# Kernel optimization log

Measured on AMD Instinct MI355X. Metric: run time of the kernel, lower is better.

The kernel has to match this reference:

```python
import jax, jax.numpy as jnp
import numpy as np

V_IN = 32000
V_OUT = 32000
E = 1024
H = 1024
B = 16
T = 512


def _lstm_layer(xs, Wih, Whh, bih, bhh):
    # xs: [T, B, in_dim]; PyTorch gate order: i, f, g, o (each size H)
    gx = jnp.einsum('tbi,gi->tbg', xs, Wih) + bih + bhh  # [T, B, 4H]

    def step(carry, g_t):
        h, c = carry
        g = g_t + h @ Whh.T  # [B, 4H]
        i, f, gg, o = jnp.split(g, 4, axis=-1)
        i = jax.nn.sigmoid(i)
        f = jax.nn.sigmoid(f)
        gg = jnp.tanh(gg)
        o = jax.nn.sigmoid(o)
        c = f * c + i * gg
        h = o * jnp.tanh(c)
        return (h, c), h

    h0 = jnp.zeros((xs.shape[1], Whh.shape[1]), dtype=xs.dtype)
    c0 = jnp.zeros_like(h0)
    _, hs = jax.lax.scan(step, (h0, c0), gx)
    return hs  # [T, B, H]


def setup_inputs() -> dict:
    key = jax.random.key(0)
    ks = jax.random.split(key, 12)
    s_e = 1.0  # nn.Embedding default init is N(0,1)
    s_l = 1.0 / np.sqrt(H)  # LSTM/Linear uniform bound 1/sqrt(H)

    def u(k, shape):
        return jax.random.uniform(k, shape, jnp.float32, -s_l, s_l)

    return {
        'x': jax.random.randint(ks[0], (B, T), 0, V_IN),
        'emb': jax.random.normal(ks[1], (V_IN, E), jnp.float32) * s_e,
        'W_ih0': u(ks[2], (4 * H, E)),
        'W_hh0': u(ks[3], (4 * H, H)),
        'b_ih0': u(ks[4], (4 * H,)),
        'b_hh0': u(ks[5], (4 * H,)),
        'W_ih1': u(ks[6], (4 * H, H)),
        'W_hh1': u(ks[7], (4 * H, H)),
        'b_ih1': u(ks[8], (4 * H,)),
        'b_hh1': u(ks[9], (4 * H,)),
        'W_out': u(ks[10], (V_OUT, H)),
        'b_out': u(ks[11], (V_OUT,)),
    }


def reference(x, emb, W_ih0, W_hh0, b_ih0, b_hh0, W_ih1, W_hh1, b_ih1, b_hh1, W_out, b_out):
    # embedding + permute to [T, B, E]
    out = emb[x].transpose(1, 0, 2)
    out = _lstm_layer(out, W_ih0, W_hh0, b_ih0, b_hh0)
    out = _lstm_layer(out, W_ih1, W_hh1, b_ih1, b_hh1)
    logits = jnp.einsum('tbh,oh->tbo', out, W_out) + b_out
    return logits.transpose(1, 0, 2)  # [B, T, V_OUT]
```

## Files before the change

kernel.cpp:

```cpp
#include <hip/hip_runtime.h>
#include <cstdint>
#include <cstddef>

typedef __bf16 bf16;
typedef float f32x4 __attribute__((ext_vector_type(4)));
typedef bf16 bf16x8 __attribute__((ext_vector_type(8)));
typedef bf16 bf16x4 __attribute__((ext_vector_type(4)));

#define AS1 __attribute__((address_space(1)))
#define AS3 __attribute__((address_space(3)))

__device__ __forceinline__ void gload_lds16(const void* g, void* l) {
  __builtin_amdgcn_global_load_lds((AS1 void*)g, (AS3 void*)l, 16, 0, 0);
}

#define RING 8
#define FLAG_WORDS 1024

__global__ __launch_bounds__(256) void init_misc(
    const float* __restrict__ bih0, const float* __restrict__ bhh0,
    const float* __restrict__ bih1, const float* __restrict__ bhh1,
    float* __restrict__ bsum0, float* __restrict__ bsum1, unsigned* __restrict__ flags) {
  int i = blockIdx.x * 256 + threadIdx.x;
  if (i < 4096) {
    bsum0[i] = bih0[i] + bhh0[i];
    bsum1[i] = bih1[i] + bhh1[i];
  }
  if (i < FLAG_WORDS) flags[i] = 0u;
}

__global__ __launch_bounds__(256) void embed_gather(
    const int* __restrict__ x, const float* __restrict__ emb, bf16* __restrict__ xe, int T) {
  int row = blockIdx.x;
  int t = row >> 4, b = row & 15;
  int tok = x[b * T + t];
  int cix = threadIdx.x << 2;
  f32x4 v = *(const f32x4*)(emb + ((size_t)tok << 10) + cix);
  bf16x4 o;
  for (int j = 0; j < 4; ++j) o[j] = (bf16)v[j];
  *(bf16x4*)(xe + ((size_t)row << 10) + cix) = o;
}

template <int OUTMODE>
__global__ __launch_bounds__(256) void gemm_bf16(
    const bf16* __restrict__ A, const float* __restrict__ Bw,
    const float* __restrict__ bias, float* __restrict__ C,
    int M, int N, int K, int Tdim) {
  __shared__ bf16 aL[2][128 * 32];
  __shared__ bf16 bL[2][128 * 32];
  const int tid = threadIdx.x;
  const int l = tid & 63, w = tid >> 6;
  const int nbm = M >> 7;
  const int bm = blockIdx.x % nbm;
  const int bn = blockIdx.x / nbm;
  const int wr = (w >> 1) << 6, wc = (w & 1) << 6;
  const int NT = K >> 5;
  const int r16 = l & 15, kq = l >> 4;

  f32x4 acc[4][4];
  for (int m = 0; m < 4; ++m)
    for (int n = 0; n < 4; ++n) acc[m][n] = (f32x4){0.f, 0.f, 0.f, 0.f};

  for (int i = 0; i < 2; ++i) {
    int lin = tid + (i << 8);
    int r = lin >> 2, s = lin & 3, c = s ^ (r & 3);
    gload_lds16(A + (size_t)((bm << 7) + r) * K + (c << 3), &aL[0][lin << 3]);
  }
  for (int i = 0; i < 2; ++i) {
    int lin = tid + (i << 8);
    int r = lin >> 2, c = lin & 3;
    const float* src = Bw + (size_t)((bn << 7) + r) * K + (c << 3);
    f32x4 v0 = *(const f32x4*)src;
    f32x4 v1 = *(const f32x4*)(src + 4);
    bf16x8 o;
    for (int j = 0; j < 4; ++j) { o[j] = (bf16)v0[j]; o[j + 4] = (bf16)v1[j]; }
    *(bf16x8*)&bL[0][(r << 5) + ((c ^ (r & 3)) << 3)] = o;
  }
  __syncthreads();

  for (int kt = 0; kt < NT; ++kt) {
    const int cur = kt & 1;
    const bool pf = (kt + 1 < NT);
    f32x4 bv0[2], bv1[2];
    int br_[2], bs_[2];
    if (pf) {
      for (int i = 0; i < 2; ++i) {
        int lin = tid + (i << 8);
        int r = lin >> 2, s = lin & 3, c = s ^ (r & 3);
        gload_lds16(A + (size_t)((bm << 7) + r) * K + ((kt + 1) << 5) + (c << 3),
                    &aL[cur ^ 1][lin << 3]);
      }
      for (int i = 0; i < 2; ++i) {
        int lin = tid + (i << 8);
        int r = lin >> 2, c = lin & 3;
        const float* src = Bw + (size_t)((bn << 7) + r) * K + ((kt + 1) << 5) + (c << 3);
        bv0[i] = *(const f32x4*)src;
        bv1[i] = *(const f32x4*)(src + 4);
        br_[i] = r;
        bs_[i] = c ^ (r & 3);
      }
    }
    bf16x8 af[4], bfr[4];
    for (int m = 0; m < 4; ++m) {
      int row = wr + (m << 4) + r16;
      int ch = kq ^ (row & 3);
      af[m] = *(const bf16x8*)&aL[cur][(row << 5) + (ch << 3)];
    }
    for (int n = 0; n < 4; ++n) {
      int row = wc + (n << 4) + r16;
      int ch = kq ^ (row & 3);
      bfr[n] = *(const bf16x8*)&bL[cur][(row << 5) + (ch << 3)];
    }
    for (int m = 0; m < 4; ++m)
      for (int n = 0; n < 4; ++n)
        acc[m][n] = __builtin_amdgcn_mfma_f32_16x16x32_bf16(af[m], bfr[n], acc[m][n], 0, 0, 0);
    if (pf) {
      for (int i = 0; i < 2; ++i) {
        bf16x8 o;
        for (int j = 0; j < 4; ++j) { o[j] = (bf16)bv0[i][j]; o[j + 4] = (bf16)bv1[i][j]; }
        *(bf16x8*)&bL[cur ^ 1][(br_[i] << 5) + (bs_[i] << 3)] = o;
      }
    }
    __syncthreads();
  }

  float bvv[4];
  for (int n = 0; n < 4; ++n) bvv[n] = bias[(bn << 7) + wc + (n << 4) + r16];
  for (int m = 0; m < 4; ++m) {
    int Rbase = (bm << 7) + wr + (m << 4) + (kq << 2);
    for (int r = 0; r < 4; ++r) {
      int R = Rbase + r;
      size_t rowoff;
      if (OUTMODE == 0) {
        rowoff = (size_t)R * N;
      } else {
        int tt = R >> 4, bb = R & 15;
        rowoff = ((size_t)bb * Tdim + tt) * N;
      }
      for (int n = 0; n < 4; ++n)
        C[rowoff + (bn << 7) + wc + (n << 4) + r16] = acc[m][n][r] + bvv[n];
    }
  }
}

__global__ __launch_bounds__(256, 1) void lstm_pipe3(
    const float* __restrict__ gx,
    const float* __restrict__ Whh0,
    const float* __restrict__ Wih1,
    const float* __restrict__ Whh1,
    const float* __restrict__ bsum1,
    bf16* __restrict__ hs0t,
    bf16* __restrict__ hs1t,
    float* __restrict__ gx1,
    bf16* __restrict__ hs1rm,
    unsigned* __restrict__ flags,
    int T) {
  __shared__ bf16 wlds[4][16 * 1024];
  __shared__ unsigned short hb[4][64];
  __shared__ unsigned tokv[4];
  const int tid = threadIdx.x;
  const int l = tid & 63, w = tid >> 6;
  const int bid = blockIdx.x;
  const int r16 = l & 15, kq = l >> 4;
  unsigned* const fL0 = flags;
  unsigned* const fB = flags + 256;
  unsigned* const fL1 = flags + 512;
  const int typ = bid >> 6;
  const int lb = bid & 63;
  const int widx = lb * 4 + w;
  const int colbase = lb * 16 + w * 4;

  {
    const float* Wsrc = (typ == 0) ? Whh0 : ((typ == 1) ? Wih1 : Whh1);
    for (int it = 0; it < 32; ++it) {
      int lin = it * 64 + l;
      int row = lin >> 7, cs = lin & 127, c = cs ^ (row & 7);
      const float* s = Wsrc + (size_t)((row >> 2) * 1024 + colbase + (row & 3)) * 1024 + c * 8;
      f32x4 v0 = *(const f32x4*)s;
      f32x4 v1 = *(const f32x4*)(s + 4);
      bf16x8 o;
      for (int j = 0; j < 4; ++j) { o[j] = (bf16)v0[j]; o[j + 4] = (bf16)v1[j]; }
      *(bf16x8*)&wlds[w][row * 1024 + cs * 8] = o;
    }
  }
  if (tid < 4) tokv[tid] = 0;
  __syncthreads();

  const int gcol = (r16 >> 2) * 1024 + colbase + (r16 & 3);
  const int b0s = (r16 >> 2) & 1, b1s = (r16 >> 3) & 1;

  auto pollq = [&](unsigned* arr, unsigned tgt) {
    unsigned* q = arr + w * 64 + (l & 15) * 4;
    for (;;) {
      unsigned a0 = __hip_atomic_load(q + 0, __ATOMIC_RELAXED, __HIP_MEMORY_SCOPE_AGENT);
      unsigned a1 = __hip_atomic_load(q + 1, __ATOMIC_RELAXED, __HIP_MEMORY_SCOPE_AGENT);
      unsigned a2 = __hip_atomic_load(q + 2, __ATOMIC_RELAXED, __HIP_MEMORY_SCOPE_AGENT);
      unsigned a3 = __hip_atomic_load(q + 3, __ATOMIC_RELAXED, __HIP_MEMORY_SCOPE_AGENT);
      if (__all(a0 >= tgt && a1 >= tgt && a2 >= tgt && a3 >= tgt)) break;
      __builtin_amdgcn_s_sleep(2);
    }
    volatile unsigned* tk = tokv;
    if (l == 0) tk[w] = tgt;
    while (tk[0] < tgt || tk[1] < tgt || tk[2] < tgt || tk[3] < tgt) {
    }
    asm volatile("" ::: "memory");
  };
  auto poll1 = [&](unsigned* p, unsigned tgt) {
    while (__hip_atomic_load(p, __ATOMIC_RELAXED, __HIP_MEMORY_SCOPE_AGENT) < tgt)
      __builtin_amdgcn_s_sleep(2);
    asm volatile("" ::: "memory");
  };
  auto chain = [&](const bf16* plane) -> f32x4 {
    f32x4 acc = (f32x4){0.f, 0.f, 0.f, 0.f};
    const char* hp = (const char*)plane;
#pragma unroll 8
    for (int kk = 0; kk < 32; ++kk) {
      int tl = kk * 8 + kq * 2;
      unsigned long long lo = *(const unsigned long long*)(hp + tl * 128 + r16 * 8);
      unsigned long long hi = *(const unsigned long long*)(hp + tl * 128 + 128 + r16 * 8);
      union { struct { unsigned long long a, b; } u; bf16x8 v; } A;
      A.u.a = lo;
      A.u.b = hi;
      bf16x8 Bf = *(const bf16x8*)&wlds[w][r16 * 1024 + (((kk * 4 + kq) ^ (r16 & 7)) << 3)];
      acc = __builtin_amdgcn_mfma_f32_16x16x32_bf16(A.v, Bf, acc, 0, 0, 0);
    }
    return acc;
  };

  if (typ == 1) {
    const float bsv = bsum1[gcol];
    unsigned* const myflag = fB + widx;
    unsigned* const partner = fL1 + widx;
    for (int t = 0; t < T; ++t) {
      if (t >= RING) poll1(partner, (unsigned)(t - RING + 1));
      pollq(fL0, (unsigned)(t + 1));
      f32x4 acc = chain(hs0t + (size_t)t * 16384);
      for (int r = 0; r < 4; ++r) acc[r] += bsv;
      float* dst = gx1 + (size_t)(t & (RING - 1)) * 65536 + widx * 256 + r16 * 16 + kq * 4;
      asm volatile("global_store_dwordx4 %0, %1, off sc0 sc1" ::"v"(dst), "v"(acc) : "memory");
      asm volatile("s_waitcnt vmcnt(0)" ::: "memory");
      if (l == 0)
        __hip_atomic_store(myflag, (unsigned)(t + 1), __ATOMIC_RELAXED, __HIP_MEMORY_SCOPE_AGENT);
    }
    return;
  }

  float cst[4] = {0.f, 0.f, 0.f, 0.f};
  unsigned* const myflag = (typ == 0) ? (fL0 + widx) : (fL1 + widx);
  unsigned* const bpartner = fB + widx;
  bf16* const houts = (typ == 0) ? hs0t : hs1t;

  for (int t = 0; t < T; ++t) {
    float gxv[4];
    if (typ == 0) {
      for (int r = 0; r < 4; ++r)
        gxv[r] = gx[(size_t)(t * 16 + kq * 4 + r) * 4096 + gcol];
    }
    if (typ == 0) {
      if (t > 0) pollq(fL0, (unsigned)t);
    } else {
      poll1(bpartner, (unsigned)(t + 1));
      if (t > 0) pollq(fL1, (unsigned)t);
    }
    f32x4 acc = (f32x4){0.f, 0.f, 0.f, 0.f};
    if (t > 0) acc = chain(houts + (size_t)(t - 1) * 16384);
    if (typ == 0) {
      for (int r = 0; r < 4; ++r) acc[r] += gxv[r];
    } else {
      const float* gp = gx1 + (size_t)(t & (RING - 1)) * 65536 + widx * 256 + r16 * 16 + kq * 4;
      f32x4 g1;
      asm volatile("global_load_dwordx4 %0, %1, off sc0 sc1\ns_waitcnt vmcnt(0)"
                   : "=v"(g1) : "v"(gp) : "memory");
      for (int r = 0; r < 4; ++r) acc[r] += g1[r];
    }
    float hv[4];
    for (int r = 0; r < 4; ++r) {
      float own = acc[r];
      float p4 = __shfl_xor(own, 4, 64);
      float ev = b0s ? p4 : own;
      float ov = b0s ? own : p4;
      float ev8 = __shfl_xor(ev, 8, 64);
      float ov8 = __shfl_xor(ov, 8, 64);
      float xi = b1s ? ev8 : ev;
      float xf = b1s ? ov8 : ov;
      float xg = b1s ? ev : ev8;
      float xo = b1s ? ov : ov8;
      float ig = 1.f / (1.f + __expf(-xi));
      float fg = 1.f / (1.f + __expf(-xf));
      float eg = __expf(2.f * xg);
      float gv = 1.f - 2.f / (eg + 1.f);
      float og = 1.f / (1.f + __expf(-xo));
      cst[r] = fg * cst[r] + ig * gv;
      float ec = __expf(2.f * cst[r]);
      float th = 1.f - 2.f / (ec + 1.f);
      hv[r] = og * th;
    }
    if (r16 < 4) {
      volatile unsigned short* hbp = hb[w];
      for (int r = 0; r < 4; ++r) {
        bf16 hbv = (bf16)hv[r];
        hbp[(kq * 4 + r) * 4 + r16] = __builtin_bit_cast(unsigned short, hbv);
      }
    }
    unsigned long long rowv = 0;
    if (l < 16) rowv = *(volatile unsigned long long*)&hb[w][l * 4];
    if (l < 16) {
      char* dst = (char*)houts + (size_t)t * 32768 + widx * 128 + l * 8;
      asm volatile("global_store_dwordx2 %0, %1, off sc0 sc1" ::"v"(dst), "v"(rowv) : "memory");
    }
    asm volatile("s_waitcnt vmcnt(0)" ::: "memory");
    if (l == 0)
      __hip_atomic_store(myflag, (unsigned)(t + 1), __ATOMIC_RELAXED, __HIP_MEMORY_SCOPE_AGENT);
    if (typ == 1 + 1 && l < 16) {
      *(unsigned long long*)((char*)hs1rm + ((size_t)(t * 16 + l) * 1024 + colbase) * 2) = rowv;
    }
  }
}

extern "C" void kernel_launch(void* const* d_in, const int* in_sizes, int n_in,
                              void* d_out, int out_size, void* d_ws, size_t ws_size,
                              hipStream_t stream) {
  const int* x = (const int*)d_in[0];
  const float* emb = (const float*)d_in[1];
  const float* Wih0 = (const float*)d_in[2];
  const float* Whh0 = (const float*)d_in[3];
  const float* bih0 = (const float*)d_in[4];
  const float* bhh0 = (const float*)d_in[5];
  const float* Wih1 = (const float*)d_in[6];
  const float* Whh1 = (const float*)d_in[7];
  const float* bih1 = (const float*)d_in[8];
  const float* bhh1 = (const float*)d_in[9];
  const float* Wout = (const float*)d_in[10];
  const float* bout = (const float*)d_in[11];

  const int T = 512, H = 1024, V = 32000;
  const int M = T * 16;
  const size_t bfb = (size_t)M * H * 2;
  const size_t out_bytes = (size_t)out_size * 4;

  char* p = (char*)d_ws;
  bf16* hs1rm = (bf16*)p;         p += bfb;
  float* bsum0 = (float*)p;       p += 4096 * 4;
  float* bsum1 = (float*)p;       p += 4096 * 4;
  unsigned* flags = (unsigned*)p; p += FLAG_WORDS * 4;

  float* gx = (float*)d_out;
  float* gx1 = (float*)((char*)d_out + (512ull << 20));
  char* tail = (char*)d_out + out_bytes - 3 * bfb;
  bf16* xe = (bf16*)tail;
  bf16* hs0t = (bf16*)(tail + bfb);
  bf16* hs1t = (bf16*)(tail + 2 * bfb);

  init_misc<<<64, 256, 0, stream>>>(bih0, bhh0, bih1, bhh1, bsum0, bsum1, flags);
  embed_gather<<<M, 256, 0, stream>>>(x, emb, xe, T);
  gemm_bf16<0><<<(M / 128) * (4096 / 128), 256, 0, stream>>>(xe, Wih0, bsum0, gx, M, 4096, H, 0);
  lstm_pipe3<<<192, 256, 0, stream>>>(gx, Whh0, Wih1, Whh1, bsum1, hs0t, hs1t, gx1, hs1rm,
                                      flags, T);
  gemm_bf16<1><<<(M / 128) * (V / 128), 256, 0, stream>>>(hs1rm, Wout, bout, (float*)d_out,
                                                          M, V, H, T);
}
```

Before: 5.294 ms.

## Fuse embedding gather into input GEMM and pre-convert W_out to bf16

The separate embedding gather kernel is removed; the first GEMM now reads token rows from the embedding table directly and converts them to bf16 while staging. When workspace allows, W_out is converted to bf16 once, so the output projection loads it straight into LDS with async global-to-LDS copies instead of fp32 register loads plus conversion. The projection GEMM also uses a grouped block ordering to improve L2 reuse and nontemporal stores for the large logits output. The added conversion pass costs extra memory traffic, and the fused gather gives up the async A-loads in the first GEMM.

```diff
diff --git a/kernel.cpp b/kernel.cpp
--- a/kernel.cpp
+++ b/kernel.cpp
@@ -5,7 +5,6 @@
 typedef __bf16 bf16;
 typedef float f32x4 __attribute__((ext_vector_type(4)));
 typedef bf16 bf16x8 __attribute__((ext_vector_type(8)));
-typedef bf16 bf16x4 __attribute__((ext_vector_type(4)));
 
 #define AS1 __attribute__((address_space(1)))
 #define AS3 __attribute__((address_space(3)))
@@ -29,77 +28,58 @@
   if (i < FLAG_WORDS) flags[i] = 0u;
 }
 
-__global__ __launch_bounds__(256) void embed_gather(
-    const int* __restrict__ x, const float* __restrict__ emb, bf16* __restrict__ xe, int T) {
-  int row = blockIdx.x;
-  int t = row >> 4, b = row & 15;
-  int tok = x[b * T + t];
-  int cix = threadIdx.x << 2;
-  f32x4 v = *(const f32x4*)(emb + ((size_t)tok << 10) + cix);
-  bf16x4 o;
-  for (int j = 0; j < 4; ++j) o[j] = (bf16)v[j];
-  *(bf16x4*)(xe + ((size_t)row << 10) + cix) = o;
-}
-
-template <int OUTMODE>
-__global__ __launch_bounds__(256) void gemm_bf16(
-    const bf16* __restrict__ A, const float* __restrict__ Bw,
-    const float* __restrict__ bias, float* __restrict__ C,
-    int M, int N, int K, int Tdim) {
-  __shared__ bf16 aL[2][128 * 32];
-  __shared__ bf16 bL[2][128 * 32];
+__global__ __launch_bounds__(256) void wout_cvt(
+    const float* __restrict__ W, bf16* __restrict__ o) {
+  size_t i = ((size_t)blockIdx.x * 256 + threadIdx.x) * 8;
+  f32x4 v0 = *(const f32x4*)(W + i);
+  f32x4 v1 = *(const f32x4*)(W + i + 4);
+  bf16x8 r;
+  for (int j = 0; j < 4; ++j) { r[j] = (bf16)v0[j]; r[j + 4] = (bf16)v1[j]; }
+  *(bf16x8*)(o + i) = r;
+}
+
+__global__ __launch_bounds__(256) void gemm_emb(
+    const int* __restrict__ x, const float* __restrict__ emb,
+    const float* __restrict__ Wih0, const float* __restrict__ bsum0,
+    float* __restrict__ C) {
+  __shared__ bf16 aL[2][4096];
+  __shared__ bf16 bL[2][4096];
   const int tid = threadIdx.x;
   const int l = tid & 63, w = tid >> 6;
-  const int nbm = M >> 7;
-  const int bm = blockIdx.x % nbm;
-  const int bn = blockIdx.x / nbm;
+  const int bm = blockIdx.x & 63;
+  const int bn = blockIdx.x >> 6;
   const int wr = (w >> 1) << 6, wc = (w & 1) << 6;
-  const int NT = K >> 5;
   const int r16 = l & 15, kq = l >> 4;
 
   f32x4 acc[4][4];
   for (int m = 0; m < 4; ++m)
     for (int n = 0; n < 4; ++n) acc[m][n] = (f32x4){0.f, 0.f, 0.f, 0.f};
 
-  for (int i = 0; i < 2; ++i) {
-    int lin = tid + (i << 8);
-    int r = lin >> 2, s = lin & 3, c = s ^ (r & 3);
-    gload_lds16(A + (size_t)((bm << 7) + r) * K + (c << 3), &aL[0][lin << 3]);
-  }
-  for (int i = 0; i < 2; ++i) {
-    int lin = tid + (i << 8);
-    int r = lin >> 2, c = lin & 3;
-    const float* src = Bw + (size_t)((bn << 7) + r) * K + (c << 3);
-    f32x4 v0 = *(const f32x4*)src;
-    f32x4 v1 = *(const f32x4*)(src + 4);
-    bf16x8 o;
-    for (int j = 0; j < 4; ++j) { o[j] = (bf16)v0[j]; o[j + 4] = (bf16)v1[j]; }
-    *(bf16x8*)&bL[0][(r << 5) + ((c ^ (r & 3)) << 3)] = o;
-  }
+  auto stage = [&](int kt, int buf) {
+    for (int i = 0; i < 2; ++i) {
+      int lin = tid + (i << 8);
+      int r = lin >> 2, c = lin & 3;
+      int rg = (bm << 7) + r;
+      int tok = x[((rg & 15) << 9) + (rg >> 4)];
+      const float* sa = emb + ((size_t)tok << 10) + (kt << 5) + (c << 3);
+      f32x4 a0 = *(const f32x4*)sa;
+      f32x4 a1 = *(const f32x4*)(sa + 4);
+      bf16x8 oa;
+      for (int j = 0; j < 4; ++j) { oa[j] = (bf16)a0[j]; oa[j + 4] = (bf16)a1[j]; }
+      *(bf16x8*)&aL[buf][(r << 5) + ((c ^ (r & 3)) << 3)] = oa;
+      const float* sb = Wih0 + (size_t)((bn << 7) + r) * 1024 + (kt << 5) + (c << 3);
+      f32x4 b0 = *(const f32x4*)sb;
+      f32x4 b1 = *(const f32x4*)(sb + 4);
+      bf16x8 ob;
+      for (int j = 0; j < 4; ++j) { ob[j] = (bf16)b0[j]; ob[j + 4] = (bf16)b1[j]; }
+      *(bf16x8*)&bL[buf][(r << 5) + ((c ^ (r & 3)) << 3)] = ob;
+    }
+  };
+  stage(0, 0);
   __syncthreads();
-
-  for (int kt = 0; kt < NT; ++kt) {
-    const int cur = kt & 1;
-    const bool pf = (kt + 1 < NT);
-    f32x4 bv0[2], bv1[2];
-    int br_[2], bs_[2];
-    if (pf) {
-      for (int i = 0; i < 2; ++i) {
-        int lin = tid + (i << 8);
-        int r = lin >> 2, s = lin & 3, c = s ^ (r & 3);
-        gload_lds16(A + (size_t)((bm << 7) + r) * K + ((kt + 1) << 5) + (c << 3),
-                    &aL[cur ^ 1][lin << 3]);
-      }
-      for (int i = 0; i < 2; ++i) {
-        int lin = tid + (i << 8);
-        int r = lin >> 2, c = lin & 3;
-        const float* src = Bw + (size_t)((bn << 7) + r) * K + ((kt + 1) << 5) + (c << 3);
-        bv0[i] = *(const f32x4*)src;
-        bv1[i] = *(const f32x4*)(src + 4);
-        br_[i] = r;
-        bs_[i] = c ^ (r & 3);
-      }
-    }
+  for (int kt = 0; kt < 32; ++kt) {
+    int cur = kt & 1;
+    if (kt + 1 < 32) stage(kt + 1, cur ^ 1);
     bf16x8 af[4], bfr[4];
     for (int m = 0; m < 4; ++m) {
       int row = wr + (m << 4) + r16;
@@ -114,7 +94,111 @@
     for (int m = 0; m < 4; ++m)
       for (int n = 0; n < 4; ++n)
         acc[m][n] = __builtin_amdgcn_mfma_f32_16x16x32_bf16(af[m], bfr[n], acc[m][n], 0, 0, 0);
+    __syncthreads();
+  }
+  float bvv[4];
+  for (int n = 0; n < 4; ++n) bvv[n] = bsum0[(bn << 7) + wc + (n << 4) + r16];
+  for (int m = 0; m < 4; ++m) {
+    int Rbase = (bm << 7) + wr + (m << 4) + (kq << 2);
+    for (int r = 0; r < 4; ++r) {
+      int R = Rbase + r;
+      size_t rowoff = (size_t)R * 4096;
+      for (int n = 0; n < 4; ++n)
+        C[rowoff + (bn << 7) + wc + (n << 4) + r16] = acc[m][n][r] + bvv[n];
+    }
+  }
+}
+
+template <bool BF16B>
+__global__ __launch_bounds__(256) void gemm_proj(
+    const bf16* __restrict__ A, const void* __restrict__ Bw_,
+    const float* __restrict__ bias, float* __restrict__ C) {
+  __shared__ bf16 aL[2][4096];
+  __shared__ bf16 bL[2][4096];
+  const int tid = threadIdx.x;
+  const int l = tid & 63, w = tid >> 6;
+  const int k = blockIdx.x % 80, sq = blockIdx.x / 80;
+  const int bm = ((sq & 7) << 3) + (k & 7);
+  const int bn = (sq >> 3) * 10 + (k >> 3);
+  const int wr = (w >> 1) << 6, wc = (w & 1) << 6;
+  const int r16 = l & 15, kq = l >> 4;
+  const bf16* Bb = (const bf16*)Bw_;
+  const float* Bf32 = (const float*)Bw_;
+
+  f32x4 acc[4][4];
+  for (int m = 0; m < 4; ++m)
+    for (int n = 0; n < 4; ++n) acc[m][n] = (f32x4){0.f, 0.f, 0.f, 0.f};
+
+  auto stageA = [&](int kt, int buf) {
+    for (int i = 0; i < 2; ++i) {
+      int lin = tid + (i << 8);
+      int r = lin >> 2, s = lin & 3, c = s ^ (r & 3);
+      gload_lds16(A + (size_t)((bm << 7) + r) * 1024 + (kt << 5) + (c << 3),
+                  &aL[buf][lin << 3]);
+    }
+  };
+  stageA(0, 0);
+  if (BF16B) {
+    for (int i = 0; i < 2; ++i) {
+      int lin = tid + (i << 8);
+      int r = lin >> 2, s = lin & 3, c = s ^ (r & 3);
+      gload_lds16(Bb + (size_t)((bn << 7) + r) * 1024 + (c << 3), &bL[0][lin << 3]);
+    }
+  } else {
+    for (int i = 0; i < 2; ++i) {
+      int lin = tid + (i << 8);
+      int r = lin >> 2, c = lin & 3;
+      const float* src = Bf32 + (size_t)((bn << 7) + r) * 1024 + (c << 3);
+      f32x4 v0 = *(const f32x4*)src;
+      f32x4 v1 = *(const f32x4*)(src + 4);
+      bf16x8 o;
+      for (int j = 0; j < 4; ++j) { o[j] = (bf16)v0[j]; o[j + 4] = (bf16)v1[j]; }
+      *(bf16x8*)&bL[0][(r << 5) + ((c ^ (r & 3)) << 3)] = o;
+    }
+  }
+  __syncthreads();
+
+  for (int kt = 0; kt < 32; ++kt) {
+    const int cur = kt & 1;
+    const bool pf = (kt + 1 < 32);
+    f32x4 bv0[2], bv1[2];
+    int br_[2], bs_[2];
     if (pf) {
+      stageA(kt + 1, cur ^ 1);
+      if (BF16B) {
+        for (int i = 0; i < 2; ++i) {
+          int lin = tid + (i << 8);
+          int r = lin >> 2, s = lin & 3, c = s ^ (r & 3);
+          gload_lds16(Bb + (size_t)((bn << 7) + r) * 1024 + ((kt + 1) << 5) + (c << 3),
+                      &bL[cur ^ 1][lin << 3]);
+        }
+      } else {
+        for (int i = 0; i < 2; ++i) {
+          int lin = tid + (i << 8);
+          int r = lin >> 2, c = lin & 3;
+          const float* src = Bf32 + (size_t)((bn << 7) + r) * 1024 + ((kt + 1) << 5) + (c << 3);
+          bv0[i] = *(const f32x4*)src;
+          bv1[i] = *(const f32x4*)(src + 4);
+          br_[i] = r;
+          bs_[i] = c ^ (r & 3);
+        }
+      }
+    }
+    bf16x8 af[4], bfr[4];
+    for (int m = 0; m < 4; ++m) {
+      int row = wr + (m << 4) + r16;
+      int ch = kq ^ (row & 3);
+      af[m] = *(const bf16x8*)&aL[cur][(row << 5) + (ch << 3)];
+    }
+    for (int n = 0; n < 4; ++n) {
+      int row = wc + (n << 4) + r16;
+      int ch = kq ^ (row & 3);
+      bfr[n] = *(const bf16x8*)&bL[cur][(row << 5) + (ch << 3)];
+    }
+    for (int m = 0; m < 4; ++m)
+      for (int n = 0; n < 4; ++n)
+        acc[m][n] = __builtin_amdgcn_mfma_f32_16x16x32_bf16(af[m], bfr[n], acc[m][n], 0, 0, 0);
+    if (pf && !BF16B) {
       for (int i = 0; i < 2; ++i) {
         bf16x8 o;
         for (int j = 0; j < 4; ++j) { o[j] = (bf16)bv0[i][j]; o[j + 4] = (bf16)bv1[i][j]; }
@@ -130,15 +214,13 @@
     int Rbase = (bm << 7) + wr + (m << 4) + (kq << 2);
     for (int r = 0; r < 4; ++r) {
       int R = Rbase + r;
-      size_t rowoff;
-      if (OUTMODE == 0) {
-        rowoff = (size_t)R * N;
-      } else {
-        int tt = R >> 4, bb = R & 15;
-        rowoff = ((size_t)bb * Tdim + tt) * N;
+      int tt = R >> 4, bb = R & 15;
+      size_t rowoff = ((size_t)bb * 512 + tt) * 32000;
+      for (int n = 0; n < 4; ++n) {
+        float v = acc[m][n][r] + bvv[n];
+        float* cp = &C[rowoff + (bn << 7) + wc + (n << 4) + r16];
+        asm volatile("global_store_dword %0, %1, off nt" ::"v"(cp), "v"(v) : "memory");
       }
-      for (int n = 0; n < 4; ++n)
-        C[rowoff + (bn << 7) + wc + (n << 4) + r16] = acc[m][n][r] + bvv[n];
     }
   }
 }
@@ -311,7 +393,7 @@
     asm volatile("s_waitcnt vmcnt(0)" ::: "memory");
     if (l == 0)
       __hip_atomic_store(myflag, (unsigned)(t + 1), __ATOMIC_RELAXED, __HIP_MEMORY_SCOPE_AGENT);
-    if (typ == 1 + 1 && l < 16) {
+    if (typ == 2 && l < 16) {
       *(unsigned long long*)((char*)hs1rm + ((size_t)(t * 16 + l) * 1024 + colbase) * 2) = rowv;
     }
   }
@@ -333,29 +415,33 @@
   const float* Wout = (const float*)d_in[10];
   const float* bout = (const float*)d_in[11];
 
-  const int T = 512, H = 1024, V = 32000;
-  const int M = T * 16;
-  const size_t bfb = (size_t)M * H * 2;
+  const int T = 512, M = 8192;
+  const size_t bfb = (size_t)M * 1024 * 2;
   const size_t out_bytes = (size_t)out_size * 4;
+  const size_t woutb_bytes = (size_t)32000 * 1024 * 2;
 
   char* p = (char*)d_ws;
   bf16* hs1rm = (bf16*)p;         p += bfb;
   float* bsum0 = (float*)p;       p += 4096 * 4;
   float* bsum1 = (float*)p;       p += 4096 * 4;
   unsigned* flags = (unsigned*)p; p += FLAG_WORDS * 4;
+  size_t base_need = (size_t)(p - (char*)d_ws);
+  const bool fat = ws_size >= base_need + woutb_bytes + 256;
+  bf16* woutb = (bf16*)p;
 
   float* gx = (float*)d_out;
   float* gx1 = (float*)((char*)d_out + (512ull << 20));
-  char* tail = (char*)d_out + out_bytes - 3 * bfb;
-  bf16* xe = (bf16*)tail;
-  bf16* hs0t = (bf16*)(tail + bfb);
-  bf16* hs1t = (bf16*)(tail + 2 * bfb);
+  char* tail = (char*)d_out + out_bytes - 2 * bfb;
+  bf16* hs0t = (bf16*)tail;
+  bf16* hs1t = (bf16*)(tail + bfb);
 
   init_misc<<<64, 256, 0, stream>>>(bih0, bhh0, bih1, bhh1, bsum0, bsum1, flags);
-  embed_gather<<<M, 256, 0, stream>>>(x, emb, xe, T);
-  gemm_bf16<0><<<(M / 128) * (4096 / 128), 256, 0, stream>>>(xe, Wih0, bsum0, gx, M, 4096, H, 0);
+  if (fat) wout_cvt<<<16000, 256, 0, stream>>>(Wout, woutb);
+  gemm_emb<<<64 * 32, 256, 0, stream>>>(x, emb, Wih0, bsum0, gx);
   lstm_pipe3<<<192, 256, 0, stream>>>(gx, Whh0, Wih1, Whh1, bsum1, hs0t, hs1t, gx1, hs1rm,
                                       flags, T);
-  gemm_bf16<1><<<(M / 128) * (V / 128), 256, 0, stream>>>(hs1rm, Wout, bout, (float*)d_out,
-                                                          M, V, H, T);
-}
+  if (fat)
+    gemm_proj<true><<<16000, 256, 0, stream>>>(hs1rm, woutb, bout, (float*)d_out);
+  else
+    gemm_proj<false><<<16000, 256, 0, stream>>>(hs1rm, Wout, bout, (float*)d_out);
+}
```

New measurement: 5.069 ms. 1.04x faster.
